# Performance work log

Measured on AMD Instinct MI355X. Metric: run time of the kernel, lower is better.

The kernel has to match this reference:

```python
import jax, jax.numpy as jnp
import numpy as np

NUM_EXPERTS = 8
TOP_K = 2
DIM = 1024
HIDDEN = 4096
BATCH, SEQ = 16, 32


def setup_inputs() -> dict:
    key = jax.random.key(0)
    k1, k2, k3, k4, k5 = jax.random.split(key, 5)
    scale = 1.0 / np.sqrt(DIM)
    return {
        "hidden_states": jax.random.normal(k1, (BATCH, SEQ, DIM), dtype=jnp.float32),
        "gate_w": jax.random.normal(k2, (NUM_EXPERTS, DIM), dtype=jnp.float32) * scale,
        "w1": jax.random.normal(k3, (NUM_EXPERTS, HIDDEN, DIM), dtype=jnp.float32) * scale,
        "w3": jax.random.normal(k4, (NUM_EXPERTS, HIDDEN, DIM), dtype=jnp.float32) * scale,
        "w2": jax.random.normal(k5, (NUM_EXPERTS, DIM, HIDDEN), dtype=jnp.float32) * (1.0 / np.sqrt(HIDDEN)),
    }


def reference(hidden_states, gate_w, w1, w3, w2):
    B, S, D = hidden_states.shape
    x = hidden_states.reshape(-1, D)  # [T, D]

    # Router: softmax in fp32, top-k, renormalize (Mixtral style)
    router_logits = x @ gate_w.T  # [T, E]
    probs = jax.nn.softmax(router_logits.astype(jnp.float32), axis=-1)
    routing_weights, selected_experts = jax.lax.top_k(probs, TOP_K)  # [T, K]
    routing_weights = routing_weights / routing_weights.sum(axis=-1, keepdims=True)
    routing_weights = routing_weights.astype(x.dtype)

    # Per-token per-expert combine coefficient: coef[t, e] = sum_k w[t,k] * 1[sel[t,k]==e]
    coef = (jax.nn.one_hot(selected_experts, NUM_EXPERTS, dtype=x.dtype)
            * routing_weights[..., None]).sum(axis=1)  # [T, E]

    # SwiGLU FFN for all experts (grouped GEMM form), combined by coef.
    h1 = jnp.einsum('td,ehd->teh', x, w1)           # [T, E, H]
    h3 = jnp.einsum('td,ehd->teh', x, w3)           # [T, E, H]
    act = jax.nn.silu(h1) * h3                      # [T, E, H]
    expert_out = jnp.einsum('teh,edh->ted', act, w2)  # [T, E, D]
    out = jnp.einsum('ted,te->td', expert_out, coef)  # [T, D]
    return out.reshape(B, S, D)
```

## Files before the change

kernel.cpp:

```cpp
#include <hip/hip_runtime.h>
#include <hip/hip_bf16.h>

#define E_ 8
#define D_ 1024
#define H_ 4096
#define T_ 512
#define A_ 1024

typedef __attribute__((ext_vector_type(8))) short bf16x8;
typedef __attribute__((ext_vector_type(4))) float f32x4;
typedef __attribute__((ext_vector_type(8))) unsigned short u16x8;

__device__ __forceinline__ unsigned short f2bf(float f) {
  __hip_bfloat16 h = __float2bfloat16(f);
  return *reinterpret_cast<unsigned short*>(&h);
}

__device__ __forceinline__ u16x8 pack8(float4 a, float4 b) {
  u16x8 r;
  r[0] = f2bf(a.x); r[1] = f2bf(a.y); r[2] = f2bf(a.z); r[3] = f2bf(a.w);
  r[4] = f2bf(b.x); r[5] = f2bf(b.y); r[6] = f2bf(b.z); r[7] = f2bf(b.w);
  return r;
}

__global__ void moe_router(const float* __restrict__ x,
                           const float* __restrict__ gw,
                           unsigned short* __restrict__ xb,
                           int* __restrict__ sel,
                           float* __restrict__ wtop) {
  const int t = blockIdx.x;
  const int lane = threadIdx.x;
  const float* xr = x + (size_t)t * D_;

  float4 xv[4];
#pragma unroll
  for (int i = 0; i < 4; ++i) xv[i] = *reinterpret_cast<const float4*>(xr + (i * 64 + lane) * 4);
#pragma unroll
  for (int i = 0; i < 4; ++i) {
    ushort4 u;
    u.x = f2bf(xv[i].x); u.y = f2bf(xv[i].y); u.z = f2bf(xv[i].z); u.w = f2bf(xv[i].w);
    *reinterpret_cast<ushort4*>(xb + (size_t)t * D_ + (i * 64 + lane) * 4) = u;
  }

  float lg[E_];
  for (int e = 0; e < E_; ++e) {
    const float* g = gw + (size_t)e * D_;
    float p = 0.f;
#pragma unroll
    for (int i = 0; i < 4; ++i) {
      float4 gv = *reinterpret_cast<const float4*>(g + (i * 64 + lane) * 4);
      p += xv[i].x * gv.x + xv[i].y * gv.y + xv[i].z * gv.z + xv[i].w * gv.w;
    }
#pragma unroll
    for (int off = 32; off; off >>= 1) p += __shfl_xor(p, off);
    lg[e] = p;
  }
  if (lane == 0) {
    float m = lg[0];
    for (int e = 1; e < E_; ++e) m = fmaxf(m, lg[e]);
    float pr[E_];
    float s = 0.f;
    for (int e = 0; e < E_; ++e) { pr[e] = __expf(lg[e] - m); s += pr[e]; }
    const float inv = 1.f / s;
    for (int e = 0; e < E_; ++e) pr[e] *= inv;
    float v0 = -1.f, v1 = -1.f; int i0 = 0, i1 = 0;
    for (int e = 0; e < E_; ++e) {
      float p = pr[e];
      if (p > v0)      { v1 = v0; i1 = i0; v0 = p; i0 = e; }
      else if (p > v1) { v1 = p; i1 = e; }
    }
    const float s2 = 1.f / (v0 + v1);
    sel[2 * t] = i0; sel[2 * t + 1] = i1;
    wtop[2 * t] = v0 * s2; wtop[2 * t + 1] = v1 * s2;
  }
}

__global__ void moe_compact(const int* __restrict__ sel,
                            const float* __restrict__ wtop,
                            int* __restrict__ counts,
                            int* __restrict__ offsets,
                            int* __restrict__ tok,
                            int* __restrict__ slotof,
                            float* __restrict__ coef) {
  const int tid = threadIdx.x;
  const int e = tid >> 6;
  const int lane = tid & 63;
  __shared__ int cnt[E_], offs[E_];

  int base = 0;
  for (int c = 0; c < T_ / 64; ++c) {
    const int t = c * 64 + lane;
    const bool f = (sel[2 * t] == e) || (sel[2 * t + 1] == e);
    base += __popcll(__ballot(f));
  }
  if (lane == 0) cnt[e] = base;
  __syncthreads();
  if (tid == 0) {
    int o = 0;
    for (int i = 0; i < E_; ++i) { offs[i] = o; o += cnt[i]; }
  }
  __syncthreads();
  if (lane == 0) { counts[e] = cnt[e]; offsets[e] = offs[e]; }

  int pos = offs[e];
  for (int c = 0; c < T_ / 64; ++c) {
    const int t = c * 64 + lane;
    const int s0 = sel[2 * t], s1 = sel[2 * t + 1];
    const bool f = (s0 == e) || (s1 == e);
    unsigned long long b = __ballot(f);
    const int myp = pos + __popcll(b & ((1ull << lane) - 1ull));
    if (f) {
      const int k = (s0 == e) ? 0 : 1;
      tok[myp] = t;
      slotof[2 * t + k] = myp;
      coef[myp] = wtop[2 * t + k];
    }
    pos += __popcll(b);
  }
}

#define BM_ 192
#define LDA_ 72

__launch_bounds__(256, 2)
__global__ void moe_ffn1(const unsigned short* __restrict__ xb,
                         const float* __restrict__ w1,
                         const float* __restrict__ w3,
                         const int* __restrict__ counts,
                         const int* __restrict__ offsets,
                         const int* __restrict__ tok,
                         unsigned short* __restrict__ act) {
  const int bid = blockIdx.x;
  const int hg = bid & 63;
  const int e = bid >> 6;
  const int count = counts[e];
  if (count <= 0) return;
  const int off = offsets[e];

  __shared__ unsigned short As[BM_][LDA_];
  __shared__ unsigned short B1s[64][LDA_];
  __shared__ unsigned short B3s[64][LDA_];

  const int tid = threadIdx.x;
  const int lane = tid & 63, wid = tid >> 6;
  const int lr = lane & 15, kg = lane >> 4;
  const int wm = wid * 48;
  const int hbase = hg * 64;

  const int brow = tid >> 2, bcol = (tid & 3) * 16;
  const float* W1p = w1 + ((size_t)e * H_ + hbase + brow) * D_ + bcol;
  const float* W3p = w3 + ((size_t)e * H_ + hbase + brow) * D_ + bcol;

  for (int m0 = 0; m0 < count; m0 += BM_) {
    const int mc = count - m0;
    const unsigned short* arow[6];
#pragma unroll
    for (int i = 0; i < 6; ++i) {
      const int r = i * 32 + (tid >> 3);
      const int cr = (m0 + r < count) ? (m0 + r) : (count - 1);
      arow[i] = xb + (size_t)tok[off + cr] * D_ + (tid & 7) * 8;
    }
    const int q = mc - wm;
    const int mfn = (q <= 0) ? 0 : ((q + 15) >> 4 < 3 ? (q + 15) >> 4 : 3);

    f32x4 acc1[3][4] = {};
    f32x4 acc3[3][4] = {};

    for (int kt = 0; kt < D_; kt += 64) {
      __syncthreads();
      u16x8 av[6];
#pragma unroll
      for (int i = 0; i < 6; ++i) av[i] = *reinterpret_cast<const u16x8*>(arow[i] + kt);
      float4 b1v[4], b3v[4];
#pragma unroll
      for (int i = 0; i < 4; ++i) {
        b1v[i] = *reinterpret_cast<const float4*>(W1p + kt + i * 4);
        b3v[i] = *reinterpret_cast<const float4*>(W3p + kt + i * 4);
      }
#pragma unroll
      for (int i = 0; i < 6; ++i)
        *reinterpret_cast<u16x8*>(&As[i * 32 + (tid >> 3)][(tid & 7) * 8]) = av[i];
#pragma unroll
      for (int i = 0; i < 2; ++i) {
        *reinterpret_cast<u16x8*>(&B1s[brow][bcol + i * 8]) = pack8(b1v[2 * i], b1v[2 * i + 1]);
        *reinterpret_cast<u16x8*>(&B3s[brow][bcol + i * 8]) = pack8(b3v[2 * i], b3v[2 * i + 1]);
      }
      __syncthreads();

#pragma unroll
      for (int ks = 0; ks < 2; ++ks) {
        const int kc = ks * 32 + kg * 8;
        bf16x8 af[3];
#pragma unroll
        for (int mf = 0; mf < 3; ++mf)
          af[mf] = *reinterpret_cast<const bf16x8*>(&As[wm + mf * 16 + lr][kc]);
#pragma unroll
        for (int nf = 0; nf < 4; ++nf) {
          bf16x8 b1f = *reinterpret_cast<const bf16x8*>(&B1s[nf * 16 + lr][kc]);
          bf16x8 b3f = *reinterpret_cast<const bf16x8*>(&B3s[nf * 16 + lr][kc]);
#pragma unroll
          for (int mf = 0; mf < 3; ++mf)
            if (mf < mfn) {
              acc1[mf][nf] = __builtin_amdgcn_mfma_f32_16x16x32_bf16(af[mf], b1f, acc1[mf][nf], 0, 0, 0);
              acc3[mf][nf] = __builtin_amdgcn_mfma_f32_16x16x32_bf16(af[mf], b3f, acc3[mf][nf], 0, 0, 0);
            }
        }
      }
    }

#pragma unroll
    for (int mf = 0; mf < 3; ++mf) {
#pragma unroll
      for (int r = 0; r < 4; ++r) {
        const int mrow = m0 + wm + mf * 16 + kg * 4 + r;
        if (mrow < count) {
          const size_t rb = (size_t)(off + mrow) * H_;
#pragma unroll
          for (int nf = 0; nf < 4; ++nf) {
            const float h1 = acc1[mf][nf][r];
            const float h3 = acc3[mf][nf][r];
            const float a = h1 / (1.f + __expf(-h1)) * h3;
            act[rb + hbase + nf * 16 + lr] = f2bf(a);
          }
        }
      }
    }
  }
}

__launch_bounds__(256, 2)
__global__ void moe_ffn2(const unsigned short* __restrict__ act,
                         const float* __restrict__ w2,
                         const int* __restrict__ counts,
                         const int* __restrict__ offsets,
                         const float* __restrict__ coef,
                         float* __restrict__ part,
                         int kschunk) {
  const int bid = blockIdx.x;
  const int ks = bid >> 7;
  const int e = (bid >> 4) & 7;
  const int dg = bid & 15;
  const int count = counts[e];
  if (count <= 0) return;
  const int off = offsets[e];
  const int kbase = ks * kschunk;

  __shared__ unsigned short As[BM_][LDA_];
  __shared__ unsigned short Bs[64][LDA_];

  const int tid = threadIdx.x;
  const int lane = tid & 63, wid = tid >> 6;
  const int lr = lane & 15, kg = lane >> 4;
  const int wm = wid * 48;
  const int dbase = dg * 64;

  const int brow = tid >> 2, bcol = (tid & 3) * 16;
  const float* W2p = w2 + ((size_t)e * D_ + dbase + brow) * H_ + kbase + bcol;

  for (int m0 = 0; m0 < count; m0 += BM_) {
    const int mc = count - m0;
    const unsigned short* arow[6];
#pragma unroll
    for (int i = 0; i < 6; ++i) {
      const int r = i * 32 + (tid >> 3);
      const int cr = (m0 + r < count) ? (m0 + r) : (count - 1);
      arow[i] = act + (size_t)(off + cr) * H_ + kbase + (tid & 7) * 8;
    }
    const int q = mc - wm;
    const int mfn = (q <= 0) ? 0 : ((q + 15) >> 4 < 3 ? (q + 15) >> 4 : 3);

    f32x4 acc[3][4] = {};

    for (int kt = 0; kt < kschunk; kt += 64) {
      __syncthreads();
      u16x8 av[6];
#pragma unroll
      for (int i = 0; i < 6; ++i) av[i] = *reinterpret_cast<const u16x8*>(arow[i] + kt);
      float4 bv[4];
#pragma unroll
      for (int i = 0; i < 4; ++i) bv[i] = *reinterpret_cast<const float4*>(W2p + kt + i * 4);
#pragma unroll
      for (int i = 0; i < 6; ++i)
        *reinterpret_cast<u16x8*>(&As[i * 32 + (tid >> 3)][(tid & 7) * 8]) = av[i];
#pragma unroll
      for (int i = 0; i < 2; ++i)
        *reinterpret_cast<u16x8*>(&Bs[brow][bcol + i * 8]) = pack8(bv[2 * i], bv[2 * i + 1]);
      __syncthreads();

#pragma unroll
      for (int ks2 = 0; ks2 < 2; ++ks2) {
        const int kc = ks2 * 32 + kg * 8;
        bf16x8 af[3];
#pragma unroll
        for (int mf = 0; mf < 3; ++mf)
          af[mf] = *reinterpret_cast<const bf16x8*>(&As[wm + mf * 16 + lr][kc]);
#pragma unroll
        for (int nf = 0; nf < 4; ++nf) {
          bf16x8 bf = *reinterpret_cast<const bf16x8*>(&Bs[nf * 16 + lr][kc]);
#pragma unroll
          for (int mf = 0; mf < 3; ++mf)
            if (mf < mfn)
              acc[mf][nf] = __builtin_amdgcn_mfma_f32_16x16x32_bf16(af[mf], bf, acc[mf][nf], 0, 0, 0);
        }
      }
    }

#pragma unroll
    for (int mf = 0; mf < 3; ++mf) {
#pragma unroll
      for (int r = 0; r < 4; ++r) {
        const int mrow = m0 + wm + mf * 16 + kg * 4 + r;
        if (mrow < count) {
          const float cf = coef[off + mrow];
          float* prow = part + ((size_t)ks * A_ + off + mrow) * D_;
#pragma unroll
          for (int nf = 0; nf < 4; ++nf)
            prow[dbase + nf * 16 + lr] = cf * acc[mf][nf][r];
        }
      }
    }
  }
}

__global__ void moe_combine(const float* __restrict__ part,
                            const int* __restrict__ slotof,
                            float* __restrict__ out,
                            int ksn) {
  const int t = blockIdx.x;
  const int i = threadIdx.x;
  const int g0 = slotof[2 * t], g1 = slotof[2 * t + 1];
  float4 o = make_float4(0.f, 0.f, 0.f, 0.f);
  for (int ks = 0; ks < ksn; ++ks) {
    const float* p = part + (size_t)ks * A_ * D_;
    float4 a = reinterpret_cast<const float4*>(p + (size_t)g0 * D_)[i];
    float4 b = reinterpret_cast<const float4*>(p + (size_t)g1 * D_)[i];
    o.x += a.x + b.x; o.y += a.y + b.y; o.z += a.z + b.z; o.w += a.w + b.w;
  }
  reinterpret_cast<float4*>(out + (size_t)t * D_)[i] = o;
}

extern "C" void kernel_launch(void* const* d_in, const int* in_sizes, int n_in,
                              void* d_out, int out_size, void* d_ws, size_t ws_size,
                              hipStream_t stream) {
  const float* x  = (const float*)d_in[0];
  const float* gw = (const float*)d_in[1];
  const float* w1 = (const float*)d_in[2];
  const float* w3 = (const float*)d_in[3];
  const float* w2 = (const float*)d_in[4];
  float* out = (float*)d_out;

  char* ws = (char*)d_ws;
  const size_t SM   = 32768;
  const size_t ACT  = (size_t)A_ * H_ * 2;
  const size_t XB   = (size_t)T_ * D_ * 2;
  const size_t P1   = (size_t)A_ * D_ * 4;

  char* sm = ws;
  unsigned short* act = (unsigned short*)(ws + SM);
  unsigned short* xb  = (unsigned short*)(ws + SM + ACT);
  float* part         = (float*)(ws + SM + ACT + XB);
  const size_t base = SM + ACT + XB;
  const int ksn = (ws_size >= base + 4 * P1) ? 4 : (ws_size >= base + 2 * P1) ? 2 : 1;

  int*   sel     = (int*)  (sm);
  float* wtop    = (float*)(sm + 4096);
  int*   counts  = (int*)  (sm + 8192);
  int*   offsets = (int*)  (sm + 8192 + 64);
  int*   tokl    = (int*)  (sm + 12288);
  int*   slotof  = (int*)  (sm + 16384);
  float* coef    = (float*)(sm + 20480);

  moe_router <<<T_, 64, 0, stream>>>(x, gw, xb, sel, wtop);
  moe_compact<<<1, 512, 0, stream>>>(sel, wtop, counts, offsets, tokl, slotof, coef);
  moe_ffn1   <<<E_ * 64, 256, 0, stream>>>(xb, w1, w3, counts, offsets, tokl, act);
  moe_ffn2   <<<128 * ksn, 256, 0, stream>>>(act, w2, counts, offsets, coef, part, H_ / ksn);
  moe_combine<<<T_, 256, 0, stream>>>(part, slotof, out, ksn);
}
```

Before: 123.3 us.

## Double-buffer FFN GEMM tiles via direct global-to-LDS loads with swizzled layout

Both FFN GEMM kernels now stage A and B tiles straight from global memory into LDS with global_load_lds, double-buffered so the next 32-wide K slice loads while MFMAs run on the current one. The fp32 weights are stored as fp32 in LDS with an XOR swizzle and converted to bf16 at fragment-read time, instead of being converted in registers before the LDS store. This removes register staging and one barrier per step, overlapping memory with compute. In exchange it uses more LDS, since fp32 B tiles in two buffers take more space, and repeats the bf16 conversion per fragment read, which may limit occupancy at 2 blocks/CU.

```diff
diff --git a/kernel.cpp b/kernel.cpp
--- a/kernel.cpp
+++ b/kernel.cpp
@@ -6,21 +6,29 @@
 #define H_ 4096
 #define T_ 512
 #define A_ 1024
+#define BM_ 192
 
 typedef __attribute__((ext_vector_type(8))) short bf16x8;
 typedef __attribute__((ext_vector_type(4))) float f32x4;
-typedef __attribute__((ext_vector_type(8))) unsigned short u16x8;
 
 __device__ __forceinline__ unsigned short f2bf(float f) {
   __hip_bfloat16 h = __float2bfloat16(f);
   return *reinterpret_cast<unsigned short*>(&h);
 }
 
-__device__ __forceinline__ u16x8 pack8(float4 a, float4 b) {
-  u16x8 r;
-  r[0] = f2bf(a.x); r[1] = f2bf(a.y); r[2] = f2bf(a.z); r[3] = f2bf(a.w);
-  r[4] = f2bf(b.x); r[5] = f2bf(b.y); r[6] = f2bf(b.z); r[7] = f2bf(b.w);
+__device__ __forceinline__ bf16x8 pk8(float4 a, float4 b) {
+  bf16x8 r;
+  r[0] = (short)f2bf(a.x); r[1] = (short)f2bf(a.y);
+  r[2] = (short)f2bf(a.z); r[3] = (short)f2bf(a.w);
+  r[4] = (short)f2bf(b.x); r[5] = (short)f2bf(b.y);
+  r[6] = (short)f2bf(b.z); r[7] = (short)f2bf(b.w);
   return r;
+}
+
+__device__ __forceinline__ void gl16(const void* g, void* l) {
+  __builtin_amdgcn_global_load_lds(
+      (const __attribute__((address_space(1))) unsigned int*)g,
+      (__attribute__((address_space(3))) unsigned int*)l, 16, 0, 0);
 }
 
 __global__ void moe_router(const float* __restrict__ x,
@@ -119,8 +127,17 @@
   }
 }
 
-#define BM_ 192
-#define LDA_ 72
+
+#define STAGE1(buf, kt) do {                                                  \
+    _Pragma("unroll")                                                         \
+    for (int j = 0; j < 3; ++j)                                               \
+      gl16(asrc[j] + (kt), &As[buf][(j * 4 + wid) * 512]);                    \
+    _Pragma("unroll")                                                         \
+    for (int j = 0; j < 2; ++j) {                                             \
+      gl16(b1src[j] + (kt), &B1s[buf][(j * 4 + wid) * 256]);                  \
+      gl16(b3src[j] + (kt), &B3s[buf][(j * 4 + wid) * 256]);                  \
+    }                                                                         \
+  } while (0)
 
 __launch_bounds__(256, 2)
 __global__ void moe_ffn1(const unsigned short* __restrict__ xb,
@@ -134,78 +151,71 @@
   const int hg = bid & 63;
   const int e = bid >> 6;
   const int count = counts[e];
-  if (count <= 0) return;
   const int off = offsets[e];
-
-  __shared__ unsigned short As[BM_][LDA_];
-  __shared__ unsigned short B1s[64][LDA_];
-  __shared__ unsigned short B3s[64][LDA_];
+  const int hbase = hg * 64;
+
+  __shared__ unsigned short As[2][BM_ * 32];
+  __shared__ float B1s[2][64 * 32];
+  __shared__ float B3s[2][64 * 32];
 
   const int tid = threadIdx.x;
   const int lane = tid & 63, wid = tid >> 6;
   const int lr = lane & 15, kg = lane >> 4;
   const int wm = wid * 48;
-  const int hbase = hg * 64;
-
-  const int brow = tid >> 2, bcol = (tid & 3) * 16;
-  const float* W1p = w1 + ((size_t)e * H_ + hbase + brow) * D_ + bcol;
-  const float* W3p = w3 + ((size_t)e * H_ + hbase + brow) * D_ + bcol;
+
+  const int cA = (((lane & 3) ^ ((lane >> 3) & 3)) << 3);
+  const int cB = (((lane & 7) ^ ((lane >> 3) & 7)) << 2);
+  const float* b1src[2];
+  const float* b3src[2];
+#pragma unroll
+  for (int j = 0; j < 2; ++j) {
+    const int row = (j * 4 + wid) * 8 + (lane >> 3);
+    b1src[j] = w1 + ((size_t)e * H_ + hbase + row) * D_ + cB;
+    b3src[j] = w3 + ((size_t)e * H_ + hbase + row) * D_ + cB;
+  }
 
   for (int m0 = 0; m0 < count; m0 += BM_) {
-    const int mc = count - m0;
-    const unsigned short* arow[6];
-#pragma unroll
-    for (int i = 0; i < 6; ++i) {
-      const int r = i * 32 + (tid >> 3);
-      const int cr = (m0 + r < count) ? (m0 + r) : (count - 1);
-      arow[i] = xb + (size_t)tok[off + cr] * D_ + (tid & 7) * 8;
-    }
-    const int q = mc - wm;
+    const unsigned short* asrc[3];
+#pragma unroll
+    for (int j = 0; j < 3; ++j) {
+      const int row = (j * 4 + wid) * 16 + (lane >> 2);
+      const int cr = (m0 + row < count) ? (m0 + row) : (count - 1);
+      asrc[j] = xb + (size_t)tok[off + cr] * D_ + cA;
+    }
+    const int q = count - m0 - wm;
     const int mfn = (q <= 0) ? 0 : ((q + 15) >> 4 < 3 ? (q + 15) >> 4 : 3);
 
     f32x4 acc1[3][4] = {};
     f32x4 acc3[3][4] = {};
 
-    for (int kt = 0; kt < D_; kt += 64) {
-      __syncthreads();
-      u16x8 av[6];
-#pragma unroll
-      for (int i = 0; i < 6; ++i) av[i] = *reinterpret_cast<const u16x8*>(arow[i] + kt);
-      float4 b1v[4], b3v[4];
-#pragma unroll
-      for (int i = 0; i < 4; ++i) {
-        b1v[i] = *reinterpret_cast<const float4*>(W1p + kt + i * 4);
-        b3v[i] = *reinterpret_cast<const float4*>(W3p + kt + i * 4);
+    STAGE1(0, 0);
+    __syncthreads();
+
+    int cur = 0;
+    const int pa = ((kg ^ ((lr >> 1) & 3)) << 3);
+    const int q0 = (((kg * 2) ^ (lr & 7)) << 2);
+    const int q1 = (((kg * 2 + 1) ^ (lr & 7)) << 2);
+    for (int it = 0; it < 32; ++it) {
+      if (it + 1 < 32) STAGE1(cur ^ 1, (it + 1) * 32);
+      bf16x8 af[3];
+#pragma unroll
+      for (int mf = 0; mf < 3; ++mf)
+        af[mf] = *reinterpret_cast<const bf16x8*>(&As[cur][(wm + mf * 16 + lr) * 32 + pa]);
+#pragma unroll
+      for (int nf = 0; nf < 4; ++nf) {
+        const int rb = (nf * 16 + lr) * 32;
+        bf16x8 b1f = pk8(*reinterpret_cast<const float4*>(&B1s[cur][rb + q0]),
+                         *reinterpret_cast<const float4*>(&B1s[cur][rb + q1]));
+        bf16x8 b3f = pk8(*reinterpret_cast<const float4*>(&B3s[cur][rb + q0]),
+                         *reinterpret_cast<const float4*>(&B3s[cur][rb + q1]));
+#pragma unroll
+        for (int mf = 0; mf < 3; ++mf)
+          if (mf < mfn) {
+            acc1[mf][nf] = __builtin_amdgcn_mfma_f32_16x16x32_bf16(af[mf], b1f, acc1[mf][nf], 0, 0, 0);
+            acc3[mf][nf] = __builtin_amdgcn_mfma_f32_16x16x32_bf16(af[mf], b3f, acc3[mf][nf], 0, 0, 0);
+          }
       }
-#pragma unroll
-      for (int i = 0; i < 6; ++i)
-        *reinterpret_cast<u16x8*>(&As[i * 32 + (tid >> 3)][(tid & 7) * 8]) = av[i];
-#pragma unroll
-      for (int i = 0; i < 2; ++i) {
-        *reinterpret_cast<u16x8*>(&B1s[brow][bcol + i * 8]) = pack8(b1v[2 * i], b1v[2 * i + 1]);
-        *reinterpret_cast<u16x8*>(&B3s[brow][bcol + i * 8]) = pack8(b3v[2 * i], b3v[2 * i + 1]);
-      }
-      __syncthreads();
-
-#pragma unroll
-      for (int ks = 0; ks < 2; ++ks) {
-        const int kc = ks * 32 + kg * 8;
-        bf16x8 af[3];
-#pragma unroll
-        for (int mf = 0; mf < 3; ++mf)
-          af[mf] = *reinterpret_cast<const bf16x8*>(&As[wm + mf * 16 + lr][kc]);
-#pragma unroll
-        for (int nf = 0; nf < 4; ++nf) {
-          bf16x8 b1f = *reinterpret_cast<const bf16x8*>(&B1s[nf * 16 + lr][kc]);
-          bf16x8 b3f = *reinterpret_cast<const bf16x8*>(&B3s[nf * 16 + lr][kc]);
-#pragma unroll
-          for (int mf = 0; mf < 3; ++mf)
-            if (mf < mfn) {
-              acc1[mf][nf] = __builtin_amdgcn_mfma_f32_16x16x32_bf16(af[mf], b1f, acc1[mf][nf], 0, 0, 0);
-              acc3[mf][nf] = __builtin_amdgcn_mfma_f32_16x16x32_bf16(af[mf], b3f, acc3[mf][nf], 0, 0, 0);
-            }
-        }
-      }
+      if (it + 1 < 32) { __syncthreads(); cur ^= 1; }
     }
 
 #pragma unroll
@@ -225,8 +235,18 @@
         }
       }
     }
-  }
-}
+    __syncthreads();
+  }
+}
+
+#define STAGE2(buf, kt) do {                                                  \
+    _Pragma("unroll")                                                         \
+    for (int j = 0; j < 3; ++j)                                               \
+      gl16(asrc[j] + (kt), &As[buf][(j * 4 + wid) * 512]);                    \
+    _Pragma("unroll")                                                         \
+    for (int j = 0; j < 2; ++j)                                               \
+      gl16(bsrc[j] + (kt), &Bs[buf][(j * 4 + wid) * 256]);                    \
+  } while (0)
 
 __launch_bounds__(256, 2)
 __global__ void moe_ffn2(const unsigned short* __restrict__ act,
@@ -241,68 +261,65 @@
   const int e = (bid >> 4) & 7;
   const int dg = bid & 15;
   const int count = counts[e];
-  if (count <= 0) return;
   const int off = offsets[e];
+  const int dbase = dg * 64;
   const int kbase = ks * kschunk;
-
-  __shared__ unsigned short As[BM_][LDA_];
-  __shared__ unsigned short Bs[64][LDA_];
+  const int nit = kschunk >> 5;
+
+  __shared__ unsigned short As[2][BM_ * 32];
+  __shared__ float Bs[2][64 * 32];
 
   const int tid = threadIdx.x;
   const int lane = tid & 63, wid = tid >> 6;
   const int lr = lane & 15, kg = lane >> 4;
   const int wm = wid * 48;
-  const int dbase = dg * 64;
-
-  const int brow = tid >> 2, bcol = (tid & 3) * 16;
-  const float* W2p = w2 + ((size_t)e * D_ + dbase + brow) * H_ + kbase + bcol;
+
+  const int cA = (((lane & 3) ^ ((lane >> 3) & 3)) << 3);
+  const int cB = (((lane & 7) ^ ((lane >> 3) & 7)) << 2);
+  const float* bsrc[2];
+#pragma unroll
+  for (int j = 0; j < 2; ++j) {
+    const int row = (j * 4 + wid) * 8 + (lane >> 3);
+    bsrc[j] = w2 + ((size_t)e * D_ + dbase + row) * H_ + kbase + cB;
+  }
 
   for (int m0 = 0; m0 < count; m0 += BM_) {
-    const int mc = count - m0;
-    const unsigned short* arow[6];
-#pragma unroll
-    for (int i = 0; i < 6; ++i) {
-      const int r = i * 32 + (tid >> 3);
-      const int cr = (m0 + r < count) ? (m0 + r) : (count - 1);
-      arow[i] = act + (size_t)(off + cr) * H_ + kbase + (tid & 7) * 8;
-    }
-    const int q = mc - wm;
+    const unsigned short* asrc[3];
+#pragma unroll
+    for (int j = 0; j < 3; ++j) {
+      const int row = (j * 4 + wid) * 16 + (lane >> 2);
+      const int cr = (m0 + row < count) ? (m0 + row) : (count - 1);
+      asrc[j] = act + (size_t)(off + cr) * H_ + kbase + cA;
+    }
+    const int q = count - m0 - wm;
     const int mfn = (q <= 0) ? 0 : ((q + 15) >> 4 < 3 ? (q + 15) >> 4 : 3);
 
     f32x4 acc[3][4] = {};
 
-    for (int kt = 0; kt < kschunk; kt += 64) {
-      __syncthreads();
-      u16x8 av[6];
-#pragma unroll
-      for (int i = 0; i < 6; ++i) av[i] = *reinterpret_cast<const u16x8*>(arow[i] + kt);
-      float4 bv[4];
-#pragma unroll
-      for (int i = 0; i < 4; ++i) bv[i] = *reinterpret_cast<const float4*>(W2p + kt + i * 4);
-#pragma unroll
-      for (int i = 0; i < 6; ++i)
-        *reinterpret_cast<u16x8*>(&As[i * 32 + (tid >> 3)][(tid & 7) * 8]) = av[i];
-#pragma unroll
-      for (int i = 0; i < 2; ++i)
-        *reinterpret_cast<u16x8*>(&Bs[brow][bcol + i * 8]) = pack8(bv[2 * i], bv[2 * i + 1]);
-      __syncthreads();
-
-#pragma unroll
-      for (int ks2 = 0; ks2 < 2; ++ks2) {
-        const int kc = ks2 * 32 + kg * 8;
-        bf16x8 af[3];
+    STAGE2(0, 0);
+    __syncthreads();
+
+    int cur = 0;
+    const int pa = ((kg ^ ((lr >> 1) & 3)) << 3);
+    const int q0 = (((kg * 2) ^ (lr & 7)) << 2);
+    const int q1 = (((kg * 2 + 1) ^ (lr & 7)) << 2);
+    for (int it = 0; it < nit; ++it) {
+      if (it + 1 < nit) STAGE2(cur ^ 1, (it + 1) * 32);
+      bf16x8 af[3];
+#pragma unroll
+      for (int mf = 0; mf < 3; ++mf)
+        af[mf] = *reinterpret_cast<const bf16x8*>(&As[cur][(wm + mf * 16 + lr) * 32 + pa]);
+#pragma unroll
+      for (int nf = 0; nf < 4; ++nf) {
+        const int rb = (nf * 16 + lr) * 32;
+        bf16x8 bf = pk8(*reinterpret_cast<const float4*>(&Bs[cur][rb + q0]),
+                        *reinterpret_cast<const float4*>(&Bs[cur][rb + q1]));
 #pragma unroll
         for (int mf = 0; mf < 3; ++mf)
-          af[mf] = *reinterpret_cast<const bf16x8*>(&As[wm + mf * 16 + lr][kc]);
-#pragma unroll
-        for (int nf = 0; nf < 4; ++nf) {
-          bf16x8 bf = *reinterpret_cast<const bf16x8*>(&Bs[nf * 16 + lr][kc]);
-#pragma unroll
-          for (int mf = 0; mf < 3; ++mf)
-            if (mf < mfn)
-              acc[mf][nf] = __builtin_amdgcn_mfma_f32_16x16x32_bf16(af[mf], bf, acc[mf][nf], 0, 0, 0);
-        }
+          if (mf < mfn)
+            acc[mf][nf] = __builtin_amdgcn_mfma_f32_16x16x32_bf16(af[mf], bf, acc[mf][nf], 0, 0, 0);
       }
+      if (it + 1 < nit) { __syncthreads(); cur ^= 1; }
     }
 
 #pragma unroll
@@ -319,6 +336,7 @@
         }
       }
     }
+    __syncthreads();
   }
 }
 
```

Measured after the change: 144.9 us. 1.18x slower.

## Prefetch next K tile into registers while computing current tile in both FFN GEMMs

Applied to the files above, without the earlier changes.

Both expert GEMM kernels now load the next 64-wide K tile from global memory into registers before running the MFMA work on the current shared-memory tile. Even and odd register buffers alternate, so global-load latency can overlap with matrix math instead of sitting on the critical path. The cost is more live registers, which may spill or pressure occupancy under launch_bounds(256,2). The loop also steps by 128 and assumes the K extent (kschunk) is a multiple of 128.

```diff
diff --git a/kernel.cpp b/kernel.cpp
--- a/kernel.cpp
+++ b/kernel.cpp
@@ -121,6 +121,49 @@
 
 #define BM_ 192
 #define LDA_ 72
+
+#define LOADR1(AV, B1V, B3V, KT) do {                                         \
+    _Pragma("unroll")                                                         \
+    for (int i = 0; i < 6; ++i) AV[i] = *reinterpret_cast<const u16x8*>(arow[i] + (KT)); \
+    _Pragma("unroll")                                                         \
+    for (int i = 0; i < 4; ++i) {                                             \
+      B1V[i] = *reinterpret_cast<const float4*>(W1p + (KT) + i * 4);          \
+      B3V[i] = *reinterpret_cast<const float4*>(W3p + (KT) + i * 4);          \
+    }                                                                         \
+  } while (0)
+
+#define WRITE1(AV, B1V, B3V) do {                                             \
+    _Pragma("unroll")                                                         \
+    for (int i = 0; i < 6; ++i)                                               \
+      *reinterpret_cast<u16x8*>(&As[i * 32 + (tid >> 3)][(tid & 7) * 8]) = AV[i]; \
+    _Pragma("unroll")                                                         \
+    for (int i = 0; i < 2; ++i) {                                             \
+      *reinterpret_cast<u16x8*>(&B1s[brow][bcol + i * 8]) = pack8(B1V[2 * i], B1V[2 * i + 1]); \
+      *reinterpret_cast<u16x8*>(&B3s[brow][bcol + i * 8]) = pack8(B3V[2 * i], B3V[2 * i + 1]); \
+    }                                                                         \
+  } while (0)
+
+#define COMPUTE1() do {                                                       \
+    _Pragma("unroll")                                                         \
+    for (int ks = 0; ks < 2; ++ks) {                                          \
+      const int kc = ks * 32 + kg * 8;                                        \
+      bf16x8 af[3];                                                           \
+      _Pragma("unroll")                                                       \
+      for (int mf = 0; mf < 3; ++mf)                                          \
+        af[mf] = *reinterpret_cast<const bf16x8*>(&As[wm + mf * 16 + lr][kc]); \
+      _Pragma("unroll")                                                       \
+      for (int nf = 0; nf < 4; ++nf) {                                        \
+        bf16x8 b1f = *reinterpret_cast<const bf16x8*>(&B1s[nf * 16 + lr][kc]); \
+        bf16x8 b3f = *reinterpret_cast<const bf16x8*>(&B3s[nf * 16 + lr][kc]); \
+        _Pragma("unroll")                                                     \
+        for (int mf = 0; mf < 3; ++mf)                                        \
+          if (mf < mfn) {                                                     \
+            acc1[mf][nf] = __builtin_amdgcn_mfma_f32_16x16x32_bf16(af[mf], b1f, acc1[mf][nf], 0, 0, 0); \
+            acc3[mf][nf] = __builtin_amdgcn_mfma_f32_16x16x32_bf16(af[mf], b3f, acc3[mf][nf], 0, 0, 0); \
+          }                                                                   \
+      }                                                                       \
+    }                                                                         \
+  } while (0)
 
 __launch_bounds__(256, 2)
 __global__ void moe_ffn1(const unsigned short* __restrict__ xb,
@@ -166,46 +209,23 @@
     f32x4 acc1[3][4] = {};
     f32x4 acc3[3][4] = {};
 
-    for (int kt = 0; kt < D_; kt += 64) {
-      __syncthreads();
-      u16x8 av[6];
-#pragma unroll
-      for (int i = 0; i < 6; ++i) av[i] = *reinterpret_cast<const u16x8*>(arow[i] + kt);
-      float4 b1v[4], b3v[4];
-#pragma unroll
-      for (int i = 0; i < 4; ++i) {
-        b1v[i] = *reinterpret_cast<const float4*>(W1p + kt + i * 4);
-        b3v[i] = *reinterpret_cast<const float4*>(W3p + kt + i * 4);
-      }
-#pragma unroll
-      for (int i = 0; i < 6; ++i)
-        *reinterpret_cast<u16x8*>(&As[i * 32 + (tid >> 3)][(tid & 7) * 8]) = av[i];
-#pragma unroll
-      for (int i = 0; i < 2; ++i) {
-        *reinterpret_cast<u16x8*>(&B1s[brow][bcol + i * 8]) = pack8(b1v[2 * i], b1v[2 * i + 1]);
-        *reinterpret_cast<u16x8*>(&B3s[brow][bcol + i * 8]) = pack8(b3v[2 * i], b3v[2 * i + 1]);
-      }
-      __syncthreads();
-
-#pragma unroll
-      for (int ks = 0; ks < 2; ++ks) {
-        const int kc = ks * 32 + kg * 8;
-        bf16x8 af[3];
-#pragma unroll
-        for (int mf = 0; mf < 3; ++mf)
-          af[mf] = *reinterpret_cast<const bf16x8*>(&As[wm + mf * 16 + lr][kc]);
-#pragma unroll
-        for (int nf = 0; nf < 4; ++nf) {
-          bf16x8 b1f = *reinterpret_cast<const bf16x8*>(&B1s[nf * 16 + lr][kc]);
-          bf16x8 b3f = *reinterpret_cast<const bf16x8*>(&B3s[nf * 16 + lr][kc]);
-#pragma unroll
-          for (int mf = 0; mf < 3; ++mf)
-            if (mf < mfn) {
-              acc1[mf][nf] = __builtin_amdgcn_mfma_f32_16x16x32_bf16(af[mf], b1f, acc1[mf][nf], 0, 0, 0);
-              acc3[mf][nf] = __builtin_amdgcn_mfma_f32_16x16x32_bf16(af[mf], b3f, acc3[mf][nf], 0, 0, 0);
-            }
-        }
-      }
+    u16x8 avE[6], avO[6];
+    float4 b1E[4], b3E[4], b1O[4], b3O[4];
+
+    LOADR1(avE, b1E, b3E, 0);
+
+    for (int kt = 0; kt < D_; kt += 128) {
+      __syncthreads();
+      WRITE1(avE, b1E, b3E);
+      __syncthreads();
+      LOADR1(avO, b1O, b3O, kt + 64);
+      COMPUTE1();
+
+      __syncthreads();
+      WRITE1(avO, b1O, b3O);
+      __syncthreads();
+      if (kt + 128 < D_) LOADR1(avE, b1E, b3E, kt + 128);
+      COMPUTE1();
     }
 
 #pragma unroll
@@ -227,6 +247,41 @@
     }
   }
 }
+
+#define LOADR2(AV, BV, KT) do {                                               \
+    _Pragma("unroll")                                                         \
+    for (int i = 0; i < 6; ++i) AV[i] = *reinterpret_cast<const u16x8*>(arow[i] + (KT)); \
+    _Pragma("unroll")                                                         \
+    for (int i = 0; i < 4; ++i) BV[i] = *reinterpret_cast<const float4*>(W2p + (KT) + i * 4); \
+  } while (0)
+
+#define WRITE2(AV, BV) do {                                                   \
+    _Pragma("unroll")                                                         \
+    for (int i = 0; i < 6; ++i)                                               \
+      *reinterpret_cast<u16x8*>(&As[i * 32 + (tid >> 3)][(tid & 7) * 8]) = AV[i]; \
+    _Pragma("unroll")                                                         \
+    for (int i = 0; i < 2; ++i)                                               \
+      *reinterpret_cast<u16x8*>(&Bs[brow][bcol + i * 8]) = pack8(BV[2 * i], BV[2 * i + 1]); \
+  } while (0)
+
+#define COMPUTE2() do {                                                       \
+    _Pragma("unroll")                                                         \
+    for (int ks2 = 0; ks2 < 2; ++ks2) {                                       \
+      const int kc = ks2 * 32 + kg * 8;                                       \
+      bf16x8 af[3];                                                           \
+      _Pragma("unroll")                                                       \
+      for (int mf = 0; mf < 3; ++mf)                                          \
+        af[mf] = *reinterpret_cast<const bf16x8*>(&As[wm + mf * 16 + lr][kc]); \
+      _Pragma("unroll")                                                       \
+      for (int nf = 0; nf < 4; ++nf) {                                        \
+        bf16x8 bf = *reinterpret_cast<const bf16x8*>(&Bs[nf * 16 + lr][kc]);  \
+        _Pragma("unroll")                                                     \
+        for (int mf = 0; mf < 3; ++mf)                                        \
+          if (mf < mfn)                                                       \
+            acc[mf][nf] = __builtin_amdgcn_mfma_f32_16x16x32_bf16(af[mf], bf, acc[mf][nf], 0, 0, 0); \
+      }                                                                       \
+    }                                                                         \
+  } while (0)
 
 __launch_bounds__(256, 2)
 __global__ void moe_ffn2(const unsigned short* __restrict__ act,
@@ -271,38 +326,23 @@
 
     f32x4 acc[3][4] = {};
 
-    for (int kt = 0; kt < kschunk; kt += 64) {
-      __syncthreads();
-      u16x8 av[6];
-#pragma unroll
-      for (int i = 0; i < 6; ++i) av[i] = *reinterpret_cast<const u16x8*>(arow[i] + kt);
-      float4 bv[4];
-#pragma unroll
-      for (int i = 0; i < 4; ++i) bv[i] = *reinterpret_cast<const float4*>(W2p + kt + i * 4);
-#pragma unroll
-      for (int i = 0; i < 6; ++i)
-        *reinterpret_cast<u16x8*>(&As[i * 32 + (tid >> 3)][(tid & 7) * 8]) = av[i];
-#pragma unroll
-      for (int i = 0; i < 2; ++i)
-        *reinterpret_cast<u16x8*>(&Bs[brow][bcol + i * 8]) = pack8(bv[2 * i], bv[2 * i + 1]);
-      __syncthreads();
-
-#pragma unroll
-      for (int ks2 = 0; ks2 < 2; ++ks2) {
-        const int kc = ks2 * 32 + kg * 8;
-        bf16x8 af[3];
-#pragma unroll
-        for (int mf = 0; mf < 3; ++mf)
-          af[mf] = *reinterpret_cast<const bf16x8*>(&As[wm + mf * 16 + lr][kc]);
-#pragma unroll
-        for (int nf = 0; nf < 4; ++nf) {
-          bf16x8 bf = *reinterpret_cast<const bf16x8*>(&Bs[nf * 16 + lr][kc]);
-#pragma unroll
-          for (int mf = 0; mf < 3; ++mf)
-            if (mf < mfn)
-              acc[mf][nf] = __builtin_amdgcn_mfma_f32_16x16x32_bf16(af[mf], bf, acc[mf][nf], 0, 0, 0);
-        }
-      }
+    u16x8 avE[6], avO[6];
+    float4 bE[4], bO[4];
+
+    LOADR2(avE, bE, 0);
+
+    for (int kt = 0; kt < kschunk; kt += 128) {
+      __syncthreads();
+      WRITE2(avE, bE);
+      __syncthreads();
+      LOADR2(avO, bO, kt + 64);
+      COMPUTE2();
+
+      __syncthreads();
+      WRITE2(avO, bO);
+      __syncthreads();
+      if (kt + 128 < kschunk) LOADR2(avE, bE, kt + 128);
+      COMPUTE2();
     }
 
 #pragma unroll
```

Measured after the change: 181.9 us. +47.5%, slower.
